# Performance work log

Hardware: AMD Instinct MI355X
Metric: run time of the kernel (lower is better)

Reference implementation:

```python
import jax, jax.numpy as jnp
import numpy as np

DIM = 768
HEADS = 12
DIM_HEAD = 64
INNER = HEADS * DIM_HEAD  # 768
EPS = 1e-5


def setup_inputs() -> dict:
    key = jax.random.key(0)
    ks = jax.random.split(key, 5)
    x = jax.random.normal(ks[0], (4, 2048, DIM), dtype=jnp.float32)
    ln_g = jnp.ones((DIM,), dtype=jnp.float32)
    ln_b = jnp.zeros((DIM,), dtype=jnp.float32)
    s1 = 1.0 / np.sqrt(DIM)
    W_qkv = jax.random.uniform(ks[1], (DIM, 3 * INNER), dtype=jnp.float32, minval=-s1, maxval=s1)
    b_qkv = jax.random.uniform(ks[2], (3 * INNER,), dtype=jnp.float32, minval=-s1, maxval=s1)
    s2 = 1.0 / np.sqrt(INNER)
    W_out = jax.random.uniform(ks[3], (INNER, DIM), dtype=jnp.float32, minval=-s2, maxval=s2)
    b_out = jax.random.uniform(ks[4], (DIM,), dtype=jnp.float32, minval=-s2, maxval=s2)
    return {"x": x, "ln_g": ln_g, "ln_b": ln_b, "W_qkv": W_qkv, "b_qkv": b_qkv, "W_out": W_out, "b_out": b_out}


def reference(x, ln_g, ln_b, W_qkv, b_qkv, W_out, b_out):
    b, n, _ = x.shape
    # pre-norm LayerNorm
    mu = jnp.mean(x, axis=-1, keepdims=True)
    var = jnp.mean(jnp.square(x - mu), axis=-1, keepdims=True)
    xn = (x - mu) * jax.lax.rsqrt(var + EPS) * ln_g + ln_b
    qkv = xn @ W_qkv + b_qkv  # [b, n, 3*inner]
    q, k, v = jnp.split(qkv, 3, axis=-1)
    def to_heads(t):
        return t.reshape(b, n, HEADS, DIM_HEAD).transpose(0, 2, 1, 3)  # b h n d
    q, k, v = map(to_heads, (q, k, v))
    q = q * (DIM_HEAD ** -0.5)
    sim = jnp.einsum('bhid,bhjd->bhij', q, k)
    attn = jax.nn.softmax(sim, axis=-1)  # dropout is identity (p=0.0)
    out = jnp.einsum('bhij,bhjd->bhid', attn, v)
    out = out.transpose(0, 2, 1, 3).reshape(b, n, INNER)
    return out @ W_out + b_out
```

## Files before the change

### kernel.cpp

```cpp
#include <hip/hip_runtime.h>
#include <cstdint>
#include <cstddef>


#define SEQ    2048
#define NBATCH 4
#define DMODEL 768
#define NHEADS 12
#define DHEAD  64
#define MROWS  (NBATCH * SEQ)
#define NQKV   (3 * DMODEL)
#define KT     64
#define NT     (SEQ / KT)

using f32x4  = __attribute__((ext_vector_type(4))) float;
using u16x8  = __attribute__((ext_vector_type(8))) unsigned short;
using s16x8  = __attribute__((ext_vector_type(8))) short;

__device__ __forceinline__ unsigned short f2bf(float f) {
  union { float f; unsigned int u; } x; x.f = f;
  unsigned int r = x.u + 0x7fffu + ((x.u >> 16) & 1u);
  return (unsigned short)(r >> 16);
}

#if defined(__has_builtin)
#if __has_builtin(__builtin_amdgcn_cvt_pk_bf16_f32)
#define HAVE_PK_BF16 1
#endif
#if __has_builtin(__builtin_amdgcn_exp2f)
#define HAVE_EXP2 1
#endif
#endif

__device__ __forceinline__ unsigned int pk_bf16(float a, float b) {
#ifdef HAVE_PK_BF16
  auto v = __builtin_amdgcn_cvt_pk_bf16_f32(a, b);
  union { decltype(v) v2; unsigned int u; } c; c.v2 = v; return c.u;
#else
  return (unsigned int)f2bf(a) | ((unsigned int)f2bf(b) << 16);
#endif
}

__device__ __forceinline__ float fexp2(float x) {
#ifdef HAVE_EXP2
  return __builtin_amdgcn_exp2f(x);
#else
  return exp2f(x);
#endif
}

__device__ __forceinline__ f32x4 mfma16(u16x8 a, u16x8 b, f32x4 c) {
  return __builtin_amdgcn_mfma_f32_16x16x32_bf16((s16x8)a, (s16x8)b, c, 0, 0, 0);
}

__device__ __forceinline__ void gl_lds16(const void* g, void* l) {
  __builtin_amdgcn_global_load_lds(
      (const __attribute__((address_space(1))) void*)g,
      (__attribute__((address_space(3))) void*)l, 16, 0, 0);
}

__global__ __launch_bounds__(256) void ln_kernel(
    const float* __restrict__ x, const float* __restrict__ g,
    const float* __restrict__ bb, unsigned short* __restrict__ xn) {
  __shared__ float red[8];
  const int row = blockIdx.x, t = threadIdx.x;
  const float* xr = x + (size_t)row * DMODEL;
  float v0 = xr[t], v1 = xr[t + 256], v2 = xr[t + 512];
  float s = v0 + v1 + v2;
#pragma unroll
  for (int o = 32; o; o >>= 1) s += __shfl_down(s, o);
  if ((t & 63) == 0) red[t >> 6] = s;
  __syncthreads();
  float mu = (red[0] + red[1] + red[2] + red[3]) * (1.0f / DMODEL);
  float d0 = v0 - mu, d1 = v1 - mu, d2 = v2 - mu;
  float q = d0 * d0 + d1 * d1 + d2 * d2;
#pragma unroll
  for (int o = 32; o; o >>= 1) q += __shfl_down(q, o);
  if ((t & 63) == 0) red[4 + (t >> 6)] = q;
  __syncthreads();
  float var = (red[4] + red[5] + red[6] + red[7]) * (1.0f / DMODEL);
  float rstd = rsqrtf(var + 1e-5f);
  size_t base = (size_t)row * DMODEL;
  xn[base + t]       = f2bf(d0 * rstd * g[t]       + bb[t]);
  xn[base + t + 256] = f2bf(d1 * rstd * g[t + 256] + bb[t + 256]);
  xn[base + t + 512] = f2bf(d2 * rstd * g[t + 512] + bb[t + 512]);
}

__global__ __launch_bounds__(256) void tconv_kernel(
    const float* __restrict__ W, unsigned short* __restrict__ Wt, int N) {
  __shared__ float tile[32][33];
  const int n0 = blockIdx.x * 32, k0 = blockIdx.y * 32;
  const int tx = threadIdx.x & 31, ty = threadIdx.x >> 5;
#pragma unroll
  for (int r = 0; r < 4; ++r)
    tile[ty + r * 8][tx] = W[(size_t)(k0 + ty + r * 8) * N + n0 + tx];
  __syncthreads();
#pragma unroll
  for (int r = 0; r < 4; ++r)
    Wt[(size_t)(n0 + ty + r * 8) * DMODEL + k0 + tx] = f2bf(tile[tx][ty + r * 8]);
}

__global__ __launch_bounds__(256, 2) void gemm_qk_kernel(
    const unsigned short* __restrict__ Wt, const unsigned short* __restrict__ xn,
    const float* __restrict__ bias, unsigned short* __restrict__ qb,
    unsigned short* __restrict__ kb) {
  __shared__ alignas(16) unsigned short As[128 * 64];
  __shared__ alignas(16) unsigned short Bs[128 * 64];
  const int t = threadIdx.x, wid = t >> 6, l = t & 63, quad = l >> 4, ll = l & 15;
  const int a0 = blockIdx.x * 128;
  const int b0 = blockIdx.y * 128;
  const int wa = (wid >> 1) * 64, wb = (wid & 1) * 64;
  const int srow = l >> 3, sblk = (l & 7) ^ srow;
  f32x4 acc[4][4] = {};
  for (int k0 = 0; k0 < DMODEL; k0 += 64) {
#pragma unroll
    for (int cc = 0; cc < 4; ++cc) {
      int call = wid * 4 + cc;
      int r = call * 8 + srow;
      gl_lds16(Wt + (size_t)(a0 + r) * DMODEL + k0 + sblk * 8, &As[call * 512]);
      gl_lds16(xn + (size_t)(b0 + r) * DMODEL + k0 + sblk * 8, &Bs[call * 512]);
    }
    __syncthreads();
#pragma unroll
    for (int ks = 0; ks < 2; ++ks) {
      u16x8 af[4], bf[4];
#pragma unroll
      for (int i = 0; i < 4; ++i) {
        int ra = wa + i * 16 + ll, rb = wb + i * 16 + ll;
        int blk = (ks * 4 + quad) ^ (ll & 7);
        af[i] = *(const u16x8*)&As[ra * 64 + blk * 8];
        bf[i] = *(const u16x8*)&Bs[rb * 64 + blk * 8];
      }
#pragma unroll
      for (int mi = 0; mi < 4; ++mi)
#pragma unroll
        for (int ni = 0; ni < 4; ++ni)
          acc[mi][ni] = mfma16(af[mi], bf[ni], acc[mi][ni]);
    }
    __syncthreads();
  }
  const bool isq = (a0 < DMODEL);
  unsigned short* dst = isq ? qb : kb;
  const float sc = isq ? 0.18033688f : 1.0f;
#pragma unroll
  for (int mi = 0; mi < 4; ++mi) {
    int row0 = a0 + wa + mi * 16 + quad * 4;
    float4 bv = *(const float4*)&bias[row0];
    int rr = isq ? row0 : row0 - DMODEL;
    int h = rr >> 6, d0 = rr & 63;
#pragma unroll
    for (int ni = 0; ni < 4; ++ni) {
      int seq = b0 + wb + ni * 16 + ll;
      int b = seq >> 11, i = seq & 2047;
      uint2 pk;
      pk.x = pk_bf16((acc[mi][ni][0] + bv.x) * sc, (acc[mi][ni][1] + bv.y) * sc);
      pk.y = pk_bf16((acc[mi][ni][2] + bv.z) * sc, (acc[mi][ni][3] + bv.w) * sc);
      *(uint2*)&dst[(size_t)((b * NHEADS + h) * SEQ + i) * DHEAD + d0] = pk;
    }
  }
}

__global__ __launch_bounds__(256, 2) void gemm_v_kernel(
    const unsigned short* __restrict__ A, const unsigned short* __restrict__ Bt,
    const float* __restrict__ bias, unsigned short* __restrict__ vt) {
  __shared__ alignas(16) unsigned short As[128 * 64];
  __shared__ alignas(16) unsigned short Bs[128 * 64];
  const int t = threadIdx.x, wid = t >> 6, l = t & 63, quad = l >> 4, ll = l & 15;
  const int m0 = blockIdx.x * 128;
  const int n0 = 2 * DMODEL + blockIdx.y * 128;
  const int wm = (wid >> 1) * 64, wn = (wid & 1) * 64;
  const int srow = l >> 3, sblk = (l & 7) ^ srow;
  f32x4 acc[4][4] = {};
  for (int k0 = 0; k0 < DMODEL; k0 += 64) {
#pragma unroll
    for (int cc = 0; cc < 4; ++cc) {
      int call = wid * 4 + cc;
      int r = call * 8 + srow;
      gl_lds16(A  + (size_t)(m0 + r) * DMODEL + k0 + sblk * 8, &As[call * 512]);
      gl_lds16(Bt + (size_t)(n0 + r) * DMODEL + k0 + sblk * 8, &Bs[call * 512]);
    }
    __syncthreads();
#pragma unroll
    for (int ks = 0; ks < 2; ++ks) {
      u16x8 af[4], bf[4];
#pragma unroll
      for (int i = 0; i < 4; ++i) {
        int ra = wm + i * 16 + ll, rb = wn + i * 16 + ll;
        int blk = (ks * 4 + quad) ^ (ll & 7);
        af[i] = *(const u16x8*)&As[ra * 64 + blk * 8];
        bf[i] = *(const u16x8*)&Bs[rb * 64 + blk * 8];
      }
#pragma unroll
      for (int mi = 0; mi < 4; ++mi)
#pragma unroll
        for (int ni = 0; ni < 4; ++ni)
          acc[mi][ni] = mfma16(af[mi], bf[ni], acc[mi][ni]);
    }
    __syncthreads();
  }
#pragma unroll
  for (int mi = 0; mi < 4; ++mi) {
    int gm = m0 + wm + mi * 16 + quad * 4;
    int b = gm >> 11, i0 = gm & 2047;
#pragma unroll
    for (int ni = 0; ni < 4; ++ni) {
      int gn = n0 + wn + ni * 16 + ll;
      float bv = bias[gn];
      int rem = gn - 2 * DMODEL;
      int h = rem >> 6, d = rem & 63;
      int bh = b * NHEADS + h;
      uint2 pk;
      pk.x = pk_bf16(acc[mi][ni][0] + bv, acc[mi][ni][1] + bv);
      pk.y = pk_bf16(acc[mi][ni][2] + bv, acc[mi][ni][3] + bv);
      *(uint2*)&vt[((size_t)bh * DHEAD + d) * SEQ + i0] = pk;
    }
  }
}

__global__ __launch_bounds__(256, 3) void attn_kernel(
    const unsigned short* __restrict__ qbuf, const unsigned short* __restrict__ kbuf,
    const unsigned short* __restrict__ vtg, unsigned short* __restrict__ ao) {
  __shared__ alignas(16) unsigned short stage[2][2][KT * DHEAD];
  __shared__ alignas(16) unsigned short Pws[4][32 * 72];
  const int t = threadIdx.x, wid = t >> 6, l = t & 63, quad = l >> 4, ll = l & 15;
  const int qt = blockIdx.x, bh = blockIdx.y;
  const unsigned short* qg  = qbuf + ((size_t)bh * SEQ + qt * 128) * DHEAD;
  const unsigned short* kg0 = kbuf + (size_t)bh * SEQ * DHEAD;
  const unsigned short* vt0 = vtg  + (size_t)bh * DHEAD * SEQ;
  const int srow = l >> 3;
  const int sblk = (l & 7) ^ srow;

  unsigned short* Qs = &stage[0][0][0];
#pragma unroll
  for (int cc = 0; cc < 4; ++cc) {
    int call = wid * 4 + cc;
    gl_lds16(qg + (call * 8 + srow) * 64 + sblk * 8, Qs + call * 512);
  }
  __syncthreads();
  u16x8 qf[2][2];
#pragma unroll
  for (int mi = 0; mi < 2; ++mi)
#pragma unroll
    for (int ks = 0; ks < 2; ++ks) {
      int r = wid * 32 + mi * 16 + ll;
      int blk = (ks * 4 + quad) ^ (ll & 7);
      qf[mi][ks] = *(const u16x8*)&Qs[r * 64 + blk * 8];
    }
  __syncthreads();

  auto stage_tile = [&](int buf, int kt2) {
    const unsigned short* kg = kg0 + (size_t)kt2 * KT * DHEAD;
#pragma unroll
    for (int c = 0; c < 2; ++c) {
      int call = wid * 2 + c;
      int r = call * 8 + srow;
      gl_lds16(kg + r * 64 + sblk * 8, &stage[buf][0][call * 512]);
      gl_lds16(vt0 + (size_t)r * SEQ + kt2 * KT + sblk * 8, &stage[buf][1][call * 512]);
    }
  };

  f32x4 oacc[2][4] = {};
  float lsum[2] = {0.f, 0.f};
  unsigned short* Pw = Pws[wid];

  stage_tile(0, 0);
  int buf = 0;
  for (int kt2 = 0; kt2 < NT; ++kt2) {
    __syncthreads();
    if (kt2 + 1 < NT) stage_tile(buf ^ 1, kt2 + 1);
    const unsigned short* Ks = &stage[buf][0][0];
    const unsigned short* Vs = &stage[buf][1][0];

    f32x4 st[2][4] = {};
#pragma unroll
    for (int ks = 0; ks < 2; ++ks)
#pragma unroll
      for (int ni = 0; ni < 4; ++ni) {
        int r = ni * 16 + ll;
        int blk = (ks * 4 + quad) ^ (ll & 7);
        u16x8 kf = *(const u16x8*)&Ks[r * 64 + blk * 8];
        st[0][ni] = mfma16(kf, qf[0][ks], st[0][ni]);
        st[1][ni] = mfma16(kf, qf[1][ks], st[1][ni]);
      }

#pragma unroll
    for (int mi = 0; mi < 2; ++mi)
#pragma unroll
      for (int ni = 0; ni < 4; ++ni) {
        float p0 = fexp2(st[mi][ni][0]);
        float p1 = fexp2(st[mi][ni][1]);
        float p2 = fexp2(st[mi][ni][2]);
        float p3 = fexp2(st[mi][ni][3]);
        lsum[mi] += (p0 + p1) + (p2 + p3);
        uint2 pk;
        pk.x = pk_bf16(p0, p1);
        pk.y = pk_bf16(p2, p3);
        *(uint2*)&Pw[(mi * 16 + ll) * 72 + ni * 16 + quad * 4] = pk;
      }
    asm volatile("s_waitcnt lgkmcnt(0)" ::: "memory");

#pragma unroll
    for (int ks = 0; ks < 2; ++ks) {
      u16x8 pf0 = *(const u16x8*)&Pw[(ll) * 72 + ks * 32 + quad * 8];
      u16x8 pf1 = *(const u16x8*)&Pw[(16 + ll) * 72 + ks * 32 + quad * 8];
#pragma unroll
      for (int di = 0; di < 4; ++di) {
        int r = di * 16 + ll;
        int blk = (ks * 4 + quad) ^ (ll & 7);
        u16x8 vf = *(const u16x8*)&Vs[r * 64 + blk * 8];
        oacc[0][di] = mfma16(pf0, vf, oacc[0][di]);
        oacc[1][di] = mfma16(pf1, vf, oacc[1][di]);
      }
    }
    buf ^= 1;
  }

  float lsF[2];
#pragma unroll
  for (int mi = 0; mi < 2; ++mi) {
    float ls = lsum[mi];
    ls += __shfl_xor(ls, 16);
    ls += __shfl_xor(ls, 32);
    lsF[mi] = ls;
  }

  const int b = bh / NHEADS, h = bh - b * NHEADS;
#pragma unroll
  for (int mi = 0; mi < 2; ++mi) {
#pragma unroll
    for (int r = 0; r < 4; ++r) {
      float inv = 1.0f / __shfl(lsF[mi], quad * 4 + r);
      int row = qt * 128 + wid * 32 + mi * 16 + quad * 4 + r;
      size_t base = ((size_t)(b * SEQ + row)) * DMODEL + h * DHEAD;
#pragma unroll
      for (int di = 0; di < 4; ++di)
        ao[base + di * 16 + ll] = f2bf(oacc[mi][di][r] * inv);
    }
  }
}

__global__ __launch_bounds__(256, 2) void gemm_out_kernel(
    const unsigned short* __restrict__ Wt, const unsigned short* __restrict__ ao,
    const float* __restrict__ bias, float* __restrict__ out) {
  __shared__ alignas(16) unsigned short As[128 * 64];
  __shared__ alignas(16) unsigned short Bs[128 * 64];
  const int t = threadIdx.x, wid = t >> 6, l = t & 63, quad = l >> 4, ll = l & 15;
  const int a0 = blockIdx.x * 128;
  const int b0 = blockIdx.y * 128;
  const int wa = (wid >> 1) * 64, wb = (wid & 1) * 64;
  const int srow = l >> 3, sblk = (l & 7) ^ srow;
  f32x4 acc[4][4] = {};
  for (int k0 = 0; k0 < DMODEL; k0 += 64) {
#pragma unroll
    for (int cc = 0; cc < 4; ++cc) {
      int call = wid * 4 + cc;
      int r = call * 8 + srow;
      gl_lds16(Wt + (size_t)(a0 + r) * DMODEL + k0 + sblk * 8, &As[call * 512]);
      gl_lds16(ao + (size_t)(b0 + r) * DMODEL + k0 + sblk * 8, &Bs[call * 512]);
    }
    __syncthreads();
#pragma unroll
    for (int ks = 0; ks < 2; ++ks) {
      u16x8 af[4], bf[4];
#pragma unroll
      for (int i = 0; i < 4; ++i) {
        int ra = wa + i * 16 + ll, rb = wb + i * 16 + ll;
        int blk = (ks * 4 + quad) ^ (ll & 7);
        af[i] = *(const u16x8*)&As[ra * 64 + blk * 8];
        bf[i] = *(const u16x8*)&Bs[rb * 64 + blk * 8];
      }
#pragma unroll
      for (int mi = 0; mi < 4; ++mi)
#pragma unroll
        for (int ni = 0; ni < 4; ++ni)
          acc[mi][ni] = mfma16(af[mi], bf[ni], acc[mi][ni]);
    }
    __syncthreads();
  }
#pragma unroll
  for (int mi = 0; mi < 4; ++mi) {
    int row0 = a0 + wa + mi * 16 + quad * 4;
    float4 bv = *(const float4*)&bias[row0];
#pragma unroll
    for (int ni = 0; ni < 4; ++ni) {
      int seq = b0 + wb + ni * 16 + ll;
      float4 o;
      o.x = acc[mi][ni][0] + bv.x;
      o.y = acc[mi][ni][1] + bv.y;
      o.z = acc[mi][ni][2] + bv.z;
      o.w = acc[mi][ni][3] + bv.w;
      *(float4*)&out[(size_t)seq * DMODEL + row0] = o;
    }
  }
}

extern "C" void kernel_launch(void* const* d_in, const int* in_sizes, int n_in,
                              void* d_out, int out_size, void* d_ws, size_t ws_size,
                              hipStream_t stream) {
  const float* x     = (const float*)d_in[0];
  const float* ln_g  = (const float*)d_in[1];
  const float* ln_b  = (const float*)d_in[2];
  const float* W_qkv = (const float*)d_in[3];
  const float* b_qkv = (const float*)d_in[4];
  const float* W_out = (const float*)d_in[5];
  const float* b_out = (const float*)d_in[6];
  float* out = (float*)d_out;

  char* ws = (char*)d_ws;
  unsigned short* xn    = (unsigned short*)(ws);
  unsigned short* wqkvt = (unsigned short*)(ws + 12582912);
  unsigned short* woutt = (unsigned short*)(ws + 16121856);
  unsigned short* qb    = (unsigned short*)(ws + 17301504);
  unsigned short* kb    = (unsigned short*)(ws + 29884416);
  unsigned short* vt    = (unsigned short*)(ws + 42467328);
  unsigned short* ao    = xn;

  ln_kernel<<<MROWS, 256, 0, stream>>>(x, ln_g, ln_b, xn);
  tconv_kernel<<<dim3(NQKV / 32, DMODEL / 32), 256, 0, stream>>>(W_qkv, wqkvt, NQKV);
  tconv_kernel<<<dim3(DMODEL / 32, DMODEL / 32), 256, 0, stream>>>(W_out, woutt, DMODEL);
  gemm_qk_kernel<<<dim3(12, 64), 256, 0, stream>>>(wqkvt, xn, b_qkv, qb, kb);
  gemm_v_kernel<<<dim3(64, 6), 256, 0, stream>>>(xn, wqkvt, b_qkv, vt);
  attn_kernel<<<dim3(SEQ / 128, NBATCH * NHEADS), 256, 0, stream>>>(qb, kb, vt, ao);
  gemm_out_kernel<<<dim3(6, 64), 256, 0, stream>>>(woutt, ao, b_out, out);
}
```

Measured before the change: 240.8 us.

## Keep softmax probabilities in registers and compute row sums via MFMA

The attention kernel no longer writes exponentiated scores to a per-wave LDS buffer and reads them back as MFMA operands. It feeds the accumulator layout directly into 16x16x16 bf16 MFMAs, loading V fragments to match, and computes the softmax denominators with an extra MFMA against a ones vector. This removes the LDS round trip, the wait and the final shuffles. The price is twice as many smaller-K MFMA instructions, and the denominator is now summed from bf16-rounded probabilities. Block indices are also remapped so that consecutive workgroups are spread across batch-heads, presumably to improve cache or XCD locality.

```diff
diff --git a/kernel.cpp b/kernel.cpp
--- a/kernel.cpp
+++ b/kernel.cpp
@@ -16,6 +16,8 @@
 using f32x4  = __attribute__((ext_vector_type(4))) float;
 using u16x8  = __attribute__((ext_vector_type(8))) unsigned short;
 using s16x8  = __attribute__((ext_vector_type(8))) short;
+using u16x4  = __attribute__((ext_vector_type(4))) unsigned short;
+using s16x4  = __attribute__((ext_vector_type(4))) short;
 
 __device__ __forceinline__ unsigned short f2bf(float f) {
   union { float f; unsigned int u; } x; x.f = f;
@@ -29,6 +31,9 @@
 #endif
 #if __has_builtin(__builtin_amdgcn_exp2f)
 #define HAVE_EXP2 1
+#endif
+#if __has_builtin(__builtin_amdgcn_mfma_f32_16x16x16bf16_1k)
+#define HAVE_MFMA_16X16X16_BF16 1
 #endif
 #endif
 
@@ -51,6 +56,17 @@
 
 __device__ __forceinline__ f32x4 mfma16(u16x8 a, u16x8 b, f32x4 c) {
   return __builtin_amdgcn_mfma_f32_16x16x32_bf16((s16x8)a, (s16x8)b, c, 0, 0, 0);
+}
+
+__device__ __forceinline__ f32x4 mfma16k16(u16x4 a, u16x4 b, f32x4 c) {
+#ifdef HAVE_MFMA_16X16X16_BF16
+  return __builtin_amdgcn_mfma_f32_16x16x16bf16_1k((s16x4)a, (s16x4)b, c, 0, 0, 0);
+#else
+  f32x4 d;
+  asm("v_mfma_f32_16x16x16_bf16 %0, %1, %2, %3"
+      : "=v"(d) : "v"(a), "v"(b), "v"(c));
+  return d;
+#endif
 }
 
 __device__ __forceinline__ void gl_lds16(const void* g, void* l) {
@@ -221,9 +237,10 @@
     const unsigned short* __restrict__ qbuf, const unsigned short* __restrict__ kbuf,
     const unsigned short* __restrict__ vtg, unsigned short* __restrict__ ao) {
   __shared__ alignas(16) unsigned short stage[2][2][KT * DHEAD];
-  __shared__ alignas(16) unsigned short Pws[4][32 * 72];
   const int t = threadIdx.x, wid = t >> 6, l = t & 63, quad = l >> 4, ll = l & 15;
-  const int qt = blockIdx.x, bh = blockIdx.y;
+  const int Lid = blockIdx.y * 16 + blockIdx.x;
+  const int w = (Lid & 7) * 96 + (Lid >> 3);
+  const int qt = w & 15, bh = w >> 4;
   const unsigned short* qg  = qbuf + ((size_t)bh * SEQ + qt * 128) * DHEAD;
   const unsigned short* kg0 = kbuf + (size_t)bh * SEQ * DHEAD;
   const unsigned short* vt0 = vtg  + (size_t)bh * DHEAD * SEQ;
@@ -260,8 +277,8 @@
   };
 
   f32x4 oacc[2][4] = {};
-  float lsum[2] = {0.f, 0.f};
-  unsigned short* Pw = Pws[wid];
+  f32x4 osum[2] = {};
+  const u16x4 onesb = {0x3f80u, 0x3f80u, 0x3f80u, 0x3f80u};
 
   stage_tile(0, 0);
   int buf = 0;
@@ -284,52 +301,37 @@
       }
 
 #pragma unroll
-    for (int mi = 0; mi < 2; ++mi)
-#pragma unroll
-      for (int ni = 0; ni < 4; ++ni) {
+    for (int ni = 0; ni < 4; ++ni) {
+      u16x4 pf[2];
+#pragma unroll
+      for (int mi = 0; mi < 2; ++mi) {
         float p0 = fexp2(st[mi][ni][0]);
         float p1 = fexp2(st[mi][ni][1]);
         float p2 = fexp2(st[mi][ni][2]);
         float p3 = fexp2(st[mi][ni][3]);
-        lsum[mi] += (p0 + p1) + (p2 + p3);
-        uint2 pk;
-        pk.x = pk_bf16(p0, p1);
-        pk.y = pk_bf16(p2, p3);
-        *(uint2*)&Pw[(mi * 16 + ll) * 72 + ni * 16 + quad * 4] = pk;
-      }
-    asm volatile("s_waitcnt lgkmcnt(0)" ::: "memory");
-
-#pragma unroll
-    for (int ks = 0; ks < 2; ++ks) {
-      u16x8 pf0 = *(const u16x8*)&Pw[(ll) * 72 + ks * 32 + quad * 8];
-      u16x8 pf1 = *(const u16x8*)&Pw[(16 + ll) * 72 + ks * 32 + quad * 8];
+        union { uint2 u; u16x4 v; } cv;
+        cv.u.x = pk_bf16(p0, p1);
+        cv.u.y = pk_bf16(p2, p3);
+        pf[mi] = cv.v;
+        osum[mi] = mfma16k16(pf[mi], onesb, osum[mi]);
+      }
+      const int voff = (((ni * 2 + (quad >> 1)) ^ (ll & 7)) << 3) + (quad & 1) * 4;
 #pragma unroll
       for (int di = 0; di < 4; ++di) {
-        int r = di * 16 + ll;
-        int blk = (ks * 4 + quad) ^ (ll & 7);
-        u16x8 vf = *(const u16x8*)&Vs[r * 64 + blk * 8];
-        oacc[0][di] = mfma16(pf0, vf, oacc[0][di]);
-        oacc[1][di] = mfma16(pf1, vf, oacc[1][di]);
+        u16x4 vf = *(const u16x4*)&Vs[(di * 16 + ll) * 64 + voff];
+        oacc[0][di] = mfma16k16(pf[0], vf, oacc[0][di]);
+        oacc[1][di] = mfma16k16(pf[1], vf, oacc[1][di]);
       }
     }
     buf ^= 1;
   }
 
-  float lsF[2];
+  const int b = bh / NHEADS, h = bh - b * NHEADS;
 #pragma unroll
   for (int mi = 0; mi < 2; ++mi) {
-    float ls = lsum[mi];
-    ls += __shfl_xor(ls, 16);
-    ls += __shfl_xor(ls, 32);
-    lsF[mi] = ls;
-  }
-
-  const int b = bh / NHEADS, h = bh - b * NHEADS;
-#pragma unroll
-  for (int mi = 0; mi < 2; ++mi) {
 #pragma unroll
     for (int r = 0; r < 4; ++r) {
-      float inv = 1.0f / __shfl(lsF[mi], quad * 4 + r);
+      float inv = 1.0f / osum[mi][r];
       int row = qt * 128 + wid * 32 + mi * 16 + quad * 4 + r;
       size_t base = ((size_t)(b * SEQ + row)) * DMODEL + h * DHEAD;
 #pragma unroll
```

Measured after the change: 247.4 us. 2.7% more time.
